# Kernel optimization log

Measured on AMD Instinct MI355X. Metric: run time of the kernel, lower is better.

## Reference

```python
import jax, jax.numpy as jnp
import numpy as np

L = 3          # num encoder layers
H = 128        # hidden_dim
NH = 8         # num_heads
HD = H // NH   # head_dim
FF = H * 4     # ff inner dim (after GLU)
B, N = 32, 512
NUM_BINS = 50


def _linear_params(key, fan_in, fan_out):
    kw, kb = jax.random.split(key)
    lim = 1.0 / np.sqrt(fan_in)
    W = jax.random.uniform(kw, (fan_in, fan_out), jnp.float32, -lim, lim)
    b = jax.random.uniform(kb, (fan_out,), jnp.float32, -lim, lim)
    return W, b


def setup_inputs() -> dict:
    key = jax.random.key(0)
    ks = jax.random.split(key, 16)
    x = jax.random.normal(ks[0], (B, N, H), jnp.float32)
    distance_matrix = jax.random.uniform(ks[1], (B, N, N), jnp.float32)
    mask = jax.random.randint(ks[2], (B, N), 0, 2).astype(bool)

    def stack_linear(k, fan_in, fan_out):
        Ws, bs = [], []
        for l in range(L):
            W, b = _linear_params(jax.random.fold_in(k, l), fan_in, fan_out)
            Ws.append(W); bs.append(b)
        return jnp.stack(Ws), jnp.stack(bs)

    Wq, bq = stack_linear(ks[3], H, H)
    Wk, bk = stack_linear(ks[4], H, H)
    Wv, bv = stack_linear(ks[5], H, H)
    Wo, bo = stack_linear(ks[6], H, H)
    dist_emb = jax.random.normal(ks[7], (L, NUM_BINS, NH), jnp.float32)
    attn_bias = jnp.zeros((L, NH, 1, 1), jnp.float32)
    g1 = jnp.ones((L, H), jnp.float32); b1 = jnp.zeros((L, H), jnp.float32)
    g2 = jnp.ones((L, H), jnp.float32); b2 = jnp.zeros((L, H), jnp.float32)
    Wf1, bf1 = stack_linear(ks[8], H, 2 * FF)
    Wf2, bf2 = stack_linear(ks[9], FF, H)
    return dict(x=x, distance_matrix=distance_matrix, mask=mask,
                Wq=Wq, bq=bq, Wk=Wk, bk=bk, Wv=Wv, bv=bv, Wo=Wo, bo=bo,
                dist_emb=dist_emb, attn_bias=attn_bias,
                g1=g1, b1=b1, g2=g2, b2=b2,
                Wf1=Wf1, bf1=bf1, Wf2=Wf2, bf2=bf2)


def _layernorm(x, g, b, eps=1e-5):
    mu = jnp.mean(x, axis=-1, keepdims=True)
    var = jnp.var(x, axis=-1, keepdims=True)
    return (x - mu) * jax.lax.rsqrt(var + eps) * g + b


def _attention(h, bins, key_mask, Wq, bq, Wk, bk, Wv, bv, Wo, bo, dist_emb, attn_bias):
    # h: [B,N,H]; bins: [B,N,N] int; key_mask: [B,N] bool (True = masked)
    Bsz, Nn, _ = h.shape
    Q = (h @ Wq + bq).reshape(Bsz, Nn, NH, HD)
    K = (h @ Wk + bk).reshape(Bsz, Nn, NH, HD)
    V = (h @ Wv + bv).reshape(Bsz, Nn, NH, HD)
    scores = jnp.einsum('bqhd,bkhd->bhqk', Q, K) / np.sqrt(HD)
    bias = jnp.transpose(dist_emb[bins], (0, 3, 1, 2))  # [B,NH,N,N]
    scores = scores + bias + attn_bias[None]
    scores = jnp.where(key_mask[:, None, None, :], -1e9, scores)
    attn = jax.nn.softmax(scores, axis=-1)
    out = jnp.einsum('bhqk,bkhd->bqhd', attn, V).reshape(Bsz, Nn, H)
    return out @ Wo + bo


def reference(x, distance_matrix, mask, Wq, bq, Wk, bk, Wv, bv, Wo, bo,
              dist_emb, attn_bias, g1, b1, g2, b2, Wf1, bf1, Wf2, bf2):
    bins = jnp.clip((distance_matrix * 10.0).astype(jnp.int32), 0, NUM_BINS - 1)
    h = x
    for l in range(L):
        # pre-LN attention block
        a = _attention(_layernorm(h, g1[l], b1[l]), bins, mask,
                       Wq[l], bq[l], Wk[l], bk[l], Wv[l], bv[l], Wo[l], bo[l],
                       dist_emb[l], attn_bias[l])
        h = h + a
        # pre-LN GLU feed-forward
        u = _layernorm(h, g2[l], b2[l]) @ Wf1[l] + bf1[l]  # [B,N,2*FF]
        ua, ub = jnp.split(u, 2, axis=-1)
        h = h + (ua * jax.nn.sigmoid(ub)) @ Wf2[l] + bf2[l]
    return h
```

## Files before the change

### kernel.cpp

```cpp
#include <hip/hip_runtime.h>
#include <stdint.h>

#define Bq 32
#define Nq 512
#define Hq 128
#define NHq 8
#define HDq 16
#define Mq (Bq * Nq)

typedef unsigned short u16;
typedef __attribute__((ext_vector_type(8))) short short8;
typedef __attribute__((ext_vector_type(8))) _Float16 half8;
typedef __attribute__((ext_vector_type(2))) __fp16 fp16x2;
typedef __attribute__((ext_vector_type(4))) float f32x4;

__device__ __forceinline__ float bf2f(u16 v) {
    return __uint_as_float(((unsigned int)v) << 16);
}
__device__ __forceinline__ float ldin(const void* p, long idx, int bf) {
    if (bf) return bf2f(((const u16*)p)[idx]);
    return ((const float*)p)[idx];
}
__device__ __forceinline__ u16 f2bf(float v) {
    unsigned int u = __float_as_uint(v);
    return (u16)((u + 0x7FFFu + ((u >> 16) & 1u)) >> 16);
}
__device__ __forceinline__ u16 f2h(float v) {
    _Float16 h = (_Float16)v;
    return *(u16*)&h;
}
__device__ __forceinline__ unsigned pk2h(float a, float b) {
    fp16x2 c = __builtin_amdgcn_cvt_pkrtz(a, b);
    return *(unsigned*)&c;
}

__global__ void prep_kernel(const void* xraw, const void* de, const void* ab,
                            const void* mraw, int* flag, float* deo, float* abo,
                            unsigned* mbits, int n) {
    __shared__ int cnt, orA, orB, orC, orD;
    int tid = threadIdx.x;
    if (tid == 0) { cnt = 0; orA = 0; orB = 0; orC = 0; orD = 0; }
    __syncthreads();
    const u16* u = (const u16*)xraw;
    int good = 0;
    for (int i = tid; i < 1024; i += 256) {
        u16 v = u[i];
        int e = (v >> 7) & 0xFF;
        if (v == 0 || (e >= 90 && e <= 141)) good++;
    }
    atomicAdd(&cnt, good);
    const uint4* p4 = (const uint4*)mraw;
    unsigned a = 0, b = 0, c = 0, d = 0;
    for (int i = tid; i < n / 16; i += 256) {
        uint4 w = p4[i];
        unsigned all = w.x | w.y | w.z | w.w;
        a |= all & 0xFEFEFEFEu;
        b |= all & 0x0000FF00u;
        c |= all & 0xFFFFFF00u;
        d |= w.y | w.w;
    }
    if (a) atomicOr(&orA, 1);
    if (b) atomicOr(&orB, 1);
    if (c) atomicOr(&orC, 1);
    if (d) atomicOr(&orD, 1);
    __syncthreads();
    int bf = (cnt >= 900);
    if (tid == 0) *flag = bf;
    int mode;
    if (orA) mode = orB ? 3 : 4;
    else if (orC) mode = 0;
    else mode = orD ? 1 : 2;
    for (int i = tid; i < 1200; i += 256) deo[i] = ldin(de, i, bf);
    if (tid < 24) abo[tid] = ldin(ab, tid, bf);
    const unsigned char* p = (const unsigned char*)mraw;
    for (int wI = tid; wI < n / 32; wI += 256) {
        unsigned word = 0;
        for (int j = 0; j < 32; ++j) {
            int i = wI * 32 + j;
            int v;
            switch (mode) {
                case 0: v = p[i]; break;
                case 1: v = ((const int*)p)[i]; break;
                case 2: v = (int)((const long long*)p)[i]; break;
                case 3: v = ((const u16*)p)[i] != 0; break;
                default: v = (((const float*)p)[i] != 0.0f); break;
            }
            if (v) word |= 1u << j;
        }
        mbits[wI] = word;
    }
}

__global__ void kprep_kernel(const unsigned* __restrict__ mbits,
                             u16* __restrict__ kidxg, int* __restrict__ nkt,
                             unsigned* __restrict__ tmask) {
    int b = blockIdx.x;
    int lane = threadIdx.x & 63;
    int pos_base = 0;
    for (int w = 0; w < 8; ++w) {
        unsigned lo = mbits[b * 16 + 2 * w], hi = mbits[b * 16 + 2 * w + 1];
        unsigned long long word = ((unsigned long long)hi << 32) | lo;
        unsigned long long un = ~word;
        int bit = (int)((un >> lane) & 1ull);
        unsigned long long before = un & ((1ull << lane) - 1ull);
        int pos = pos_base + __popcll(before);
        if (bit) kidxg[b * 512 + pos] = (u16)(w * 64 + lane);
        pos_base += __popcll(un);
    }
    int nk = pos_base;
    int nkp = (nk + 31) & ~31;
    if (nkp == 0) nkp = 32;
    int nt = nkp >> 5;
    for (int j = nk + lane; j < nkp; j += 64) kidxg[b * 512 + j] = 0;
    if (lane == 0) {
        nkt[b] = nt;
        for (int t = 0; t < 16; ++t) tmask[b * 16 + t] = 0;
        int rem = nk & 31;
        if (rem) tmask[b * 16 + nt - 1] = 0xFFFFFFFFu << rem;
        if (nk == 0) tmask[b * 16] = 0xFFFFFFFFu;
    }
}

__global__ __launch_bounds__(256) void binsc_kernel(
    const void* __restrict__ dist, const u16* __restrict__ kidxg,
    const int* __restrict__ nkt, unsigned char* __restrict__ binsc,
    const int* flagp) {
    int bf = *flagp;
    int b = blockIdx.y;
    int q0 = blockIdx.x * 8;
    __shared__ u16 kl[512];
    __shared__ int ntS;
    int tid = threadIdx.x;
    if (tid == 0) ntS = nkt[b];
    kl[tid] = kidxg[b * 512 + tid];
    kl[tid + 256] = kidxg[b * 512 + tid + 256];
    __syncthreads();
    int nkp = ntS * 32;
    for (int rq = 0; rq < 8; ++rq) {
        int q = q0 + rq;
        long rowoff = ((long)b * 512 + q) * 512;
        for (int j = tid; j < nkp; j += 256) {
            float d = ldin(dist, rowoff + kl[j], bf);
            int v = (int)(d * 10.0f);
            v = v < 0 ? 0 : (v > 49 ? 49 : v);
            binsc[((size_t)b * 512 + q) * 512 + j] = (unsigned char)(v << 2);
        }
    }
}

__global__ __launch_bounds__(256) void init_ln_kernel(
    const void* x, float* __restrict__ h, u16* __restrict__ hn,
    const void* graw, const void* braw, const int* flagp) {
    int bf = *flagp;
    int row = blockIdx.x * 4 + (threadIdx.x >> 6);
    int lane = threadIdx.x & 63;
    float x0 = ldin(x, (long)row * Hq + lane, bf);
    float x1 = ldin(x, (long)row * Hq + lane + 64, bf);
    h[(size_t)row * Hq + lane] = x0;
    h[(size_t)row * Hq + lane + 64] = x1;
    float s = x0 + x1, s2 = x0 * x0 + x1 * x1;
#pragma unroll
    for (int o = 32; o; o >>= 1) {
        s += __shfl_xor(s, o);
        s2 += __shfl_xor(s2, o);
    }
    float mu = s * (1.0f / 128.0f);
    float var = fmaxf(s2 * (1.0f / 128.0f) - mu * mu, 0.0f);
    float rr = rsqrtf(var + 1e-5f);
    float g0 = ldin(graw, lane, bf), g1v = ldin(graw, lane + 64, bf);
    float b0 = ldin(braw, lane, bf), b1v = ldin(braw, lane + 64, bf);
    hn[(size_t)row * Hq + lane]      = f2bf((x0 - mu) * rr * g0 + b0);
    hn[(size_t)row * Hq + lane + 64] = f2bf((x1 - mu) * rr * g1v + b1v);
}

__global__ __launch_bounds__(256) void wtrans_kernel(
    const void* Wqr, const void* Wkr, const void* Wvr, const void* Wor,
    const void* Wf1r, const void* Wf2r,
    u16* qkvT, u16* oT, u16* f1T, u16* f2T, const int* flagp) {
    int bf = *flagp;
    int bid = blockIdx.x;
    int l = bid >> 8, r = bid & 255;
    const void* src; u16* dst; long soff, doff; int Kd, Nd, t;
    if (r < 64) {
        int mat = r >> 4; t = r & 15; Kd = 128; Nd = 128;
        soff = (long)l * 16384;
        if (mat == 0)      { src = Wqr; dst = qkvT; doff = (long)l * 49152; }
        else if (mat == 1) { src = Wkr; dst = qkvT; doff = (long)l * 49152 + 16384; }
        else if (mat == 2) { src = Wvr; dst = qkvT; doff = (long)l * 49152 + 32768; }
        else               { src = Wor; dst = oT;   doff = (long)l * 16384; }
    } else if (r < 192) {
        t = r - 64; Kd = 128; Nd = 1024;
        src = Wf1r; soff = (long)l * 131072; dst = f1T; doff = (long)l * 131072;
    } else {
        t = r - 192; Kd = 512; Nd = 128;
        src = Wf2r; soff = (long)l * 65536; dst = f2T; doff = (long)l * 65536;
    }
    int ntile = Nd >> 5;
    int tk = t / ntile, tn = t % ntile;
    __shared__ u16 Ts[32][33];
    int rr = threadIdx.x >> 3, cc0 = (threadIdx.x & 7) * 4;
#pragma unroll
    for (int i = 0; i < 4; ++i) {
        long idx = soff + (long)(tk * 32 + rr) * Nd + tn * 32 + cc0 + i;
        Ts[rr][cc0 + i] = f2bf(ldin(src, idx, bf));
    }
    __syncthreads();
#pragma unroll
    for (int i = 0; i < 4; ++i) {
        long idx = doff + (long)(tn * 32 + rr) * Kd + tk * 32 + cc0 + i;
        dst[idx] = Ts[cc0 + i][rr];
    }
}

__global__ __launch_bounds__(256, 2) void qkv_mfma_kernel(
    const u16* __restrict__ A, const u16* __restrict__ qkvT_l,
    const void* bqr, const void* bkr, const void* bvr, long bOff,
    u16* __restrict__ Qo, u16* __restrict__ Ko, u16* __restrict__ Vo,
    const int* flagp) {
    int sel = blockIdx.y;
    const u16* WT = qkvT_l + (size_t)sel * 16384;
    const void* braw = sel == 0 ? bqr : (sel == 1 ? bkr : bvr);
    u16* C = sel == 0 ? Qo : (sel == 1 ? Ko : Vo);
    float scale = sel == 0 ? 0.25f : 1.0f;
    __shared__ __align__(16) u16 As[64][40];
    __shared__ __align__(16) u16 Bs[128][40];
    int tid = threadIdx.x;
    int m0 = blockIdx.x * 64;
    int wave = tid >> 6, lane = tid & 63;
    int wm = (wave >> 1) * 32, wn = (wave & 1) * 64;
    int q = lane >> 4, ln = lane & 15;
    f32x4 zero = {0.f, 0.f, 0.f, 0.f};
    f32x4 acc[2][4];
#pragma unroll
    for (int i = 0; i < 2; ++i)
#pragma unroll
        for (int j = 0; j < 4; ++j) acc[i][j] = zero;
    int sar = tid >> 2, sac = (tid & 3) * 8;
    int sbr = tid >> 1, sbc = (tid & 1) * 16;
    const u16* Ap = A + (size_t)(m0 + sar) * 128 + sac;
    const u16* Bp = WT + (size_t)sbr * 128 + sbc;
#pragma unroll
    for (int k0 = 0; k0 < 128; k0 += 32) {
        uint4 av = *(const uint4*)(Ap + k0);
        uint4 b0 = *(const uint4*)(Bp + k0);
        uint4 b1 = *(const uint4*)(Bp + k0 + 8);
        *(uint4*)&As[sar][sac] = av;
        *(uint4*)&Bs[sbr][sbc] = b0; *(uint4*)&Bs[sbr][sbc + 8] = b1;
        __syncthreads();
        short8 af[2], bfv[4];
#pragma unroll
        for (int t = 0; t < 2; ++t) af[t] = *(const short8*)&As[wm + t * 16 + ln][q * 8];
#pragma unroll
        for (int t = 0; t < 4; ++t) bfv[t] = *(const short8*)&Bs[wn + t * 16 + ln][q * 8];
#pragma unroll
        for (int ti = 0; ti < 2; ++ti)
#pragma unroll
            for (int tj = 0; tj < 4; ++tj)
                acc[ti][tj] = __builtin_amdgcn_mfma_f32_16x16x32_bf16(
                    af[ti], bfv[tj], acc[ti][tj], 0, 0, 0);
        __syncthreads();
    }
    int bf = *flagp;
#pragma unroll
    for (int tj = 0; tj < 4; ++tj) {
        int n = wn + tj * 16 + ln;
        float bias = ldin(braw, bOff + n, bf);
#pragma unroll
        for (int ti = 0; ti < 2; ++ti)
#pragma unroll
            for (int r = 0; r < 4; ++r) {
                int m = m0 + wm + ti * 16 + q * 4 + r;
                C[(size_t)m * 128 + n] = f2h((acc[ti][tj][r] + bias) * scale);
            }
    }
}

__global__ __launch_bounds__(256, 1) void layer_ffn_kernel(
    const u16* __restrict__ att, const u16* __restrict__ oT_l,
    const void* __restrict__ bo, long boOff,
    float* __restrict__ h,
    const void* g2, const void* b2, long ln2Off,
    const u16* __restrict__ f1T_l, const void* __restrict__ bf1r, long bf1Off,
    const u16* __restrict__ f2T_l, const void* __restrict__ bf2r, long bf2Off,
    const void* g1, const void* b1, long ln1Off,
    u16* __restrict__ hnout, void* __restrict__ outp, const int* flagp) {
    __shared__ __align__(16) char Lds[151552];
    u16 (*As)[136]   = (u16(*)[136])Lds;
    u16 (*hn2)[136]  = (u16(*)[136])Lds;
    float (*Ct)[128] = (float(*)[128])(Lds + 17408);
    u16 (*vg)[520]   = (u16(*)[520])(Lds + 50176);
    u16 (*Bs)[136]   = (u16(*)[136])(Lds + 116736);
    u16 (*Ba)[136]   = (u16(*)[136])(Lds + 116736);
    u16 (*Bb)[136]   = (u16(*)[136])(Lds + 134144);

    int tid = threadIdx.x;
    int m0 = blockIdx.x * 64;
    int wave = tid >> 6, lane = tid & 63;
    int wm = (wave >> 1) * 32, wn = (wave & 1) * 64;
    int q = lane >> 4, ln = lane & 15;
    int bf = *flagp;
    f32x4 zero = {0.f, 0.f, 0.f, 0.f};

#pragma unroll
    for (int i = 0; i < 4; ++i) {
        int idx = tid + i * 256; int r = idx >> 4, c = (idx & 15) << 3;
        *(uint4*)&As[r][c] = *(const uint4*)(att + (size_t)(m0 + r) * 128 + c);
    }
#pragma unroll
    for (int i = 0; i < 8; ++i) {
        int idx = tid + i * 256; int r = idx >> 4, c = (idx & 15) << 3;
        *(uint4*)&Bs[r][c] = *(const uint4*)(oT_l + (size_t)r * 128 + c);
    }
    __syncthreads();
    f32x4 acc[2][4];
#pragma unroll
    for (int i = 0; i < 2; ++i)
#pragma unroll
        for (int j = 0; j < 4; ++j) acc[i][j] = zero;
#pragma unroll
    for (int kf = 0; kf < 128; kf += 32) {
        short8 af[2], bfv[4];
#pragma unroll
        for (int t = 0; t < 2; ++t)
            af[t] = *(const short8*)&As[wm + t * 16 + ln][kf + q * 8];
#pragma unroll
        for (int t = 0; t < 4; ++t)
            bfv[t] = *(const short8*)&Bs[wn + t * 16 + ln][kf + q * 8];
#pragma unroll
        for (int ti = 0; ti < 2; ++ti)
#pragma unroll
            for (int tj = 0; tj < 4; ++tj)
                acc[ti][tj] = __builtin_amdgcn_mfma_f32_16x16x32_bf16(
                    af[ti], bfv[tj], acc[ti][tj], 0, 0, 0);
    }
#pragma unroll
    for (int tj = 0; tj < 4; ++tj) {
        int n = wn + tj * 16 + ln;
        float bias = ldin(bo, boOff + n, bf);
#pragma unroll
        for (int ti = 0; ti < 2; ++ti)
#pragma unroll
            for (int r = 0; r < 4; ++r) {
                int lm = wm + ti * 16 + q * 4 + r;
                Ct[lm][n] = acc[ti][tj][r] + bias + h[(size_t)(m0 + lm) * 128 + n];
            }
    }
    __syncthreads();
    {
        float gg0 = ldin(g2, ln2Off + lane, bf), gg1 = ldin(g2, ln2Off + lane + 64, bf);
        float bb0 = ldin(b2, ln2Off + lane, bf), bb1 = ldin(b2, ln2Off + lane + 64, bf);
        for (int rr = 0; rr < 16; ++rr) {
            int row = wave * 16 + rr;
            float x0 = Ct[row][lane], x1 = Ct[row][lane + 64];
            float s = x0 + x1, s2v = x0 * x0 + x1 * x1;
#pragma unroll
            for (int o = 32; o; o >>= 1) {
                s += __shfl_xor(s, o);
                s2v += __shfl_xor(s2v, o);
            }
            float mu = s * (1.0f / 128.0f);
            float var = fmaxf(s2v * (1.0f / 128.0f) - mu * mu, 0.0f);
            float rstd = rsqrtf(var + 1e-5f);
            hn2[row][lane]      = f2bf((x0 - mu) * rstd * gg0 + bb0);
            hn2[row][lane + 64] = f2bf((x1 - mu) * rstd * gg1 + bb1);
        }
    }
    int wn2 = (wave & 1) * 32;
    uint4 ra[4], rb[4];
#pragma unroll
    for (int i = 0; i < 4; ++i) {
        int idx = tid + i * 256; int r = idx >> 4, c = (idx & 15) << 3;
        ra[i] = *(const uint4*)(f1T_l + (size_t)r * 128 + c);
        rb[i] = *(const uint4*)(f1T_l + (size_t)(512 + r) * 128 + c);
    }
    for (int ch = 0; ch < 8; ++ch) {
#pragma unroll
        for (int i = 0; i < 4; ++i) {
            int idx = tid + i * 256; int r = idx >> 4, c = (idx & 15) << 3;
            *(uint4*)&Ba[r][c] = ra[i];
            *(uint4*)&Bb[r][c] = rb[i];
        }
        if (ch < 7) {
            int n0 = (ch + 1) * 64;
#pragma unroll
            for (int i = 0; i < 4; ++i) {
                int idx = tid + i * 256; int r = idx >> 4, c = (idx & 15) << 3;
                ra[i] = *(const uint4*)(f1T_l + (size_t)(n0 + r) * 128 + c);
                rb[i] = *(const uint4*)(f1T_l + (size_t)(512 + n0 + r) * 128 + c);
            }
        }
        __syncthreads();
        f32x4 aA[2][2], aB[2][2];
#pragma unroll
        for (int i = 0; i < 2; ++i)
#pragma unroll
            for (int j = 0; j < 2; ++j) { aA[i][j] = zero; aB[i][j] = zero; }
#pragma unroll
        for (int kf = 0; kf < 128; kf += 32) {
            short8 af[2], bav[2], bbv[2];
#pragma unroll
            for (int t = 0; t < 2; ++t)
                af[t] = *(const short8*)&hn2[wm + t * 16 + ln][kf + q * 8];
#pragma unroll
            for (int t = 0; t < 2; ++t) {
                bav[t] = *(const short8*)&Ba[wn2 + t * 16 + ln][kf + q * 8];
                bbv[t] = *(const short8*)&Bb[wn2 + t * 16 + ln][kf + q * 8];
            }
#pragma unroll
            for (int ti = 0; ti < 2; ++ti)
#pragma unroll
                for (int tj = 0; tj < 2; ++tj) {
                    aA[ti][tj] = __builtin_amdgcn_mfma_f32_16x16x32_bf16(
                        af[ti], bav[tj], aA[ti][tj], 0, 0, 0);
                    aB[ti][tj] = __builtin_amdgcn_mfma_f32_16x16x32_bf16(
                        af[ti], bbv[tj], aB[ti][tj], 0, 0, 0);
                }
        }
        int n0 = ch * 64;
#pragma unroll
        for (int tj = 0; tj < 2; ++tj) {
            int n = n0 + wn2 + tj * 16 + ln;
            float bA = ldin(bf1r, bf1Off + n, bf);
            float bB = ldin(bf1r, bf1Off + 512 + n, bf);
#pragma unroll
            for (int ti = 0; ti < 2; ++ti)
#pragma unroll
                for (int r = 0; r < 4; ++r) {
                    int lm = wm + ti * 16 + q * 4 + r;
                    float ua = aA[ti][tj][r] + bA;
                    float ub = aB[ti][tj][r] + bB;
                    vg[lm][n] = f2bf(ua / (1.0f + __expf(-ub)));
                }
        }
        __syncthreads();
    }
    uint4 rf[8];
#pragma unroll
    for (int i = 0; i < 8; ++i) {
        int idx = tid + i * 256; int r = idx >> 4, c = (idx & 15) << 3;
        rf[i] = *(const uint4*)(f2T_l + (size_t)r * 512 + c);
    }
    f32x4 accF[2][4];
#pragma unroll
    for (int i = 0; i < 2; ++i)
#pragma unroll
        for (int j = 0; j < 4; ++j) accF[i][j] = zero;
    for (int ch = 0; ch < 4; ++ch) {
#pragma unroll
        for (int i = 0; i < 8; ++i) {
            int idx = tid + i * 256; int r = idx >> 4, c = (idx & 15) << 3;
            *(uint4*)&Bs[r][c] = rf[i];
        }
        if (ch < 3) {
            int k0 = (ch + 1) * 128;
#pragma unroll
            for (int i = 0; i < 8; ++i) {
                int idx = tid + i * 256; int r = idx >> 4, c = (idx & 15) << 3;
                rf[i] = *(const uint4*)(f2T_l + (size_t)r * 512 + k0 + c);
            }
        }
        __syncthreads();
#pragma unroll
        for (int kf = 0; kf < 128; kf += 32) {
            short8 af[2], bfv[4];
#pragma unroll
            for (int t = 0; t < 2; ++t)
                af[t] = *(const short8*)&vg[wm + t * 16 + ln][ch * 128 + kf + q * 8];
#pragma unroll
            for (int t = 0; t < 4; ++t)
                bfv[t] = *(const short8*)&Bs[wn + t * 16 + ln][kf + q * 8];
#pragma unroll
            for (int ti = 0; ti < 2; ++ti)
#pragma unroll
                for (int tj = 0; tj < 4; ++tj)
                    accF[ti][tj] = __builtin_amdgcn_mfma_f32_16x16x32_bf16(
                        af[ti], bfv[tj], accF[ti][tj], 0, 0, 0);
        }
        __syncthreads();
    }
#pragma unroll
    for (int tj = 0; tj < 4; ++tj) {
        int n = wn + tj * 16 + ln;
        float bias = ldin(bf2r, bf2Off + n, bf);
#pragma unroll
        for (int ti = 0; ti < 2; ++ti)
#pragma unroll
            for (int r = 0; r < 4; ++r) {
                int lm = wm + ti * 16 + q * 4 + r;
                float v = accF[ti][tj][r] + bias + Ct[lm][n];
                h[(size_t)(m0 + lm) * 128 + n] = v;
                Ct[lm][n] = v;
                if (outp) {
                    if (bf) ((u16*)outp)[(size_t)(m0 + lm) * 128 + n] = f2bf(v);
                    else ((float*)outp)[(size_t)(m0 + lm) * 128 + n] = v;
                }
            }
    }
    if (hnout) {
        __syncthreads();
        float gg0 = ldin(g1, ln1Off + lane, bf), gg1 = ldin(g1, ln1Off + lane + 64, bf);
        float bb0 = ldin(b1, ln1Off + lane, bf), bb1 = ldin(b1, ln1Off + lane + 64, bf);
        for (int rr = 0; rr < 16; ++rr) {
            int row = wave * 16 + rr;
            float x0 = Ct[row][lane], x1 = Ct[row][lane + 64];
            float s = x0 + x1, s2v = x0 * x0 + x1 * x1;
#pragma unroll
            for (int o = 32; o; o >>= 1) {
                s += __shfl_xor(s, o);
                s2v += __shfl_xor(s2v, o);
            }
            float mu = s * (1.0f / 128.0f);
            float var = fmaxf(s2v * (1.0f / 128.0f) - mu * mu, 0.0f);
            float rstd = rsqrtf(var + 1e-5f);
            hnout[(size_t)(m0 + row) * 128 + lane]      = f2bf((x0 - mu) * rstd * gg0 + bb0);
            hnout[(size_t)(m0 + row) * 128 + lane + 64] = f2bf((x1 - mu) * rstd * gg1 + bb1);
        }
    }
}

__global__ __launch_bounds__(256, 4) void attn_kernel(
    const u16* __restrict__ Qh, const u16* __restrict__ Kh,
    const u16* __restrict__ Vh, const unsigned char* __restrict__ binsc,
    const u16* __restrict__ kidxg, const int* __restrict__ nktp,
    const unsigned* __restrict__ tmaskp, const float* __restrict__ deL,
    const float* __restrict__ abL, u16* __restrict__ out) {
    int id = blockIdx.x;
    int c = id & 7, t5 = id >> 3;
    int nh = t5 & 7;
    int pair = ((t5 >> 3) << 3) | c;
    int b = pair >> 2, qq = pair & 3;

    __shared__ __align__(16) u16 KsF[8192];
    __shared__ __align__(16) u16 VT[16 * 520];
    __shared__ __align__(16) u16 Pl[4 * 16 * 40];

    int tid = threadIdx.x;
    int nt = __builtin_amdgcn_readfirstlane(nktp[b]);
    int nkp = nt * 32;
    const u16* Kp = Kh + (size_t)(b * Nq) * Hq + nh * HDq;
    const u16* Vp = Vh + (size_t)(b * Nq) * Hq + nh * HDq;
    for (int r = tid; r < nkp; r += 256) {
        int row = kidxg[b * 512 + r];
        int kt = r >> 5, s = (r >> 4) & 1, lnr = r & 15;
        uint4 k0v = *(const uint4*)(Kp + (size_t)row * Hq);
        uint4 k1v = *(const uint4*)(Kp + (size_t)row * Hq + 8);
        *(uint4*)&KsF[kt * 512 + s * 256 + lnr * 8]       = k0v;
        *(uint4*)&KsF[kt * 512 + s * 256 + 128 + lnr * 8] = k1v;
        uint4 v0 = *(const uint4*)(Vp + (size_t)row * Hq);
        uint4 v1 = *(const uint4*)(Vp + (size_t)row * Hq + 8);
        u16 vv[16];
        *(uint4*)&vv[0] = v0; *(uint4*)&vv[8] = v1;
#pragma unroll
        for (int d = 0; d < 16; ++d) VT[d * 520 + r] = vv[d];
    }
    __syncthreads();

    int wave = tid >> 6, lane = tid & 63;
    int quad = lane >> 4, ln = lane & 15;
    int q0w = qq * 128 + wave * 32;

    float tblf = (lane < 50) ? deL[lane * NHq + nh] + abL[nh] : 0.0f;
    int tbli = __float_as_int(tblf);
    unsigned tl = tmaskp[b * 16 + nt - 1];

    half8 qf[2];
#pragma unroll
    for (int t = 0; t < 2; ++t) {
        uint4 qv = {0, 0, 0, 0};
        if (quad < 2)
            qv = *(const uint4*)(Qh + (size_t)(b * Nq + q0w + t * 16 + ln) * Hq
                                 + nh * HDq + quad * 8);
        qf[t] = *(half8*)&qv;
    }

    f32x4 zero = {0.f, 0.f, 0.f, 0.f};
    f32x4 acc[2] = {zero, zero};
    float zp[2] = {0.f, 0.f};
    _Float16* Pw = (_Float16*)&Pl[wave * 640];
    const _Float16* KsH = (const _Float16*)KsF;
    const _Float16* VTH = (const _Float16*)VT;
    const unsigned char* brow0 = binsc + ((size_t)b * 512 + (q0w + ln)) * 512;
    const unsigned char* brow1 = brow0 + (size_t)16 * 512;

    unsigned pb00 = *(const unsigned*)(brow0 + quad * 4);
    unsigned pb01 = *(const unsigned*)(brow0 + 16 + quad * 4);
    unsigned pb10 = *(const unsigned*)(brow1 + quad * 4);
    unsigned pb11 = *(const unsigned*)(brow1 + 16 + quad * 4);

    for (int kt = 0; kt < nt; ++kt) {
        int k0 = kt * 32;
        unsigned w = (kt == nt - 1) ? tl : 0u;
        unsigned cb00 = pb00, cb01 = pb01, cb10 = pb10, cb11 = pb11;
        if (kt < nt - 1) {
            pb00 = *(const unsigned*)(brow0 + k0 + 32 + quad * 4);
            pb01 = *(const unsigned*)(brow0 + k0 + 48 + quad * 4);
            pb10 = *(const unsigned*)(brow1 + k0 + 32 + quad * 4);
            pb11 = *(const unsigned*)(brow1 + k0 + 48 + quad * 4);
        }
        half8 vb = *(const half8*)(VTH + ln * 520 + k0 + quad * 8);
        half8 ka0 = {}, ka1 = {};
        if (quad < 2) {
            ka0 = *(const half8*)(KsH + kt * 512 + quad * 128 + ln * 8);
            ka1 = *(const half8*)(KsH + kt * 512 + 256 + quad * 128 + ln * 8);
        }
#pragma unroll
        for (int t = 0; t < 2; ++t) {
            unsigned bw0 = t == 0 ? cb00 : cb10;
            unsigned bw1 = t == 0 ? cb01 : cb11;
            f32x4 s0 = __builtin_amdgcn_mfma_f32_16x16x32_f16(ka0, qf[t], zero, 0, 0, 0);
            f32x4 s1 = __builtin_amdgcn_mfma_f32_16x16x32_f16(ka1, qf[t], zero, 0, 0, 0);
            float p[8];
#pragma unroll
            for (int r = 0; r < 4; ++r) {
                float bias = __int_as_float(__builtin_amdgcn_ds_bpermute(
                    (int)((bw0 >> (8 * r)) & 0xFFu), tbli));
                float sc = s0[r] + bias;
                bool m = (w >> (quad * 4 + r)) & 1u;
                p[r] = m ? 0.0f : __expf(sc);
            }
#pragma unroll
            for (int r = 0; r < 4; ++r) {
                float bias = __int_as_float(__builtin_amdgcn_ds_bpermute(
                    (int)((bw1 >> (8 * r)) & 0xFFu), tbli));
                float sc = s1[r] + bias;
                bool m = (w >> (16 + quad * 4 + r)) & 1u;
                p[4 + r] = m ? 0.0f : __expf(sc);
            }
            zp[t] += ((p[0] + p[1]) + (p[2] + p[3])) +
                     ((p[4] + p[5]) + (p[6] + p[7]));
            uint2 w0, w1;
            w0.x = pk2h(p[0], p[1]); w0.y = pk2h(p[2], p[3]);
            w1.x = pk2h(p[4], p[5]); w1.y = pk2h(p[6], p[7]);
            *(uint2*)(Pw + ln * 40 + quad * 4)      = w0;
            *(uint2*)(Pw + ln * 40 + 16 + quad * 4) = w1;
            half8 pa = *(const half8*)(Pw + ln * 40 + quad * 8);
            acc[t] = __builtin_amdgcn_mfma_f32_16x16x32_f16(pa, vb, acc[t], 0, 0, 0);
        }
    }
#pragma unroll
    for (int t = 0; t < 2; ++t) {
        zp[t] += __shfl_xor(zp[t], 16);
        zp[t] += __shfl_xor(zp[t], 32);
    }
#pragma unroll
    for (int t = 0; t < 2; ++t) {
#pragma unroll
        for (int r = 0; r < 4; ++r) {
            float zz = __shfl(zp[t], quad * 4 + r);
            float val = acc[t][r] / fmaxf(zz, 1e-35f);
            int qrow = q0w + t * 16 + quad * 4 + r;
            out[(size_t)(b * Nq + qrow) * Hq + nh * HDq + ln] = f2bf(val);
        }
    }
}

extern "C" void kernel_launch(void* const* d_in, const int* in_sizes, int n_in,
                              void* d_out, int out_size, void* d_ws, size_t ws_size,
                              hipStream_t stream) {
    const void* x  = d_in[0];
    const void* dist = d_in[1];
    const void* mask = d_in[2];
    const void* Wq = d_in[3];  const void* bq = d_in[4];
    const void* Wk = d_in[5];  const void* bk = d_in[6];
    const void* Wv = d_in[7];  const void* bv = d_in[8];
    const void* Wo = d_in[9];  const void* bo = d_in[10];
    const void* de = d_in[11]; const void* ab = d_in[12];
    const void* g1 = d_in[13]; const void* b1 = d_in[14];
    const void* g2 = d_in[15]; const void* b2 = d_in[16];
    const void* Wf1 = d_in[17]; const void* bf1 = d_in[18];
    const void* Wf2 = d_in[19]; const void* bf2 = d_in[20];

    char* ws = (char*)d_ws;
    const size_t OFF_DE   = 64;
    const size_t OFF_AB   = 5120;
    const size_t OFF_BINS = 8192;
    const size_t OFF_MSK  = OFF_BINS + 8388608;
    const size_t OFF_KIDX = OFF_MSK + 4096;
    const size_t OFF_NKT  = OFF_KIDX + 32768;
    const size_t OFF_TM   = OFF_NKT + 256;
    const size_t OFF_H    = OFF_TM + 4096;
    const size_t OFF_QKV  = OFF_H + 8388608;
    const size_t OFF_HN   = OFF_QKV + 25165824;
    const size_t OFF_ATT  = OFF_HN + 4194304;
    const size_t OFF_WT   = OFF_ATT + 4194304;
    const size_t NEEDED   = OFF_WT + 1572864;
    if (ws_size < NEEDED) return;

    int* flag = (int*)ws;
    float* deF = (float*)(ws + OFF_DE);
    float* abF = (float*)(ws + OFF_AB);
    unsigned char* binsc = (unsigned char*)(ws + OFF_BINS);
    unsigned* mbits = (unsigned*)(ws + OFF_MSK);
    u16* kidxg = (u16*)(ws + OFF_KIDX);
    int* nkt = (int*)(ws + OFF_NKT);
    unsigned* tmask = (unsigned*)(ws + OFF_TM);
    float* h = (float*)(ws + OFF_H);
    u16* Qh = (u16*)(ws + OFF_QKV);
    u16* Kh = Qh + 2097152;
    u16* Vh = Qh + 2 * 2097152;
    u16* hn = (u16*)(ws + OFF_HN);
    u16* att = (u16*)(ws + OFF_ATT);
    u16* qkvT = (u16*)(ws + OFF_WT);
    u16* oT  = qkvT + 147456;
    u16* f1T = oT + 49152;
    u16* f2T = f1T + 393216;

    prep_kernel<<<1, 256, 0, stream>>>(x, de, ab, mask, flag, deF, abF, mbits, Bq * Nq);
    kprep_kernel<<<32, 64, 0, stream>>>(mbits, kidxg, nkt, tmask);
    dim3 gbc(64, 32);
    binsc_kernel<<<gbc, 256, 0, stream>>>(dist, kidxg, nkt, binsc, flag);
    init_ln_kernel<<<4096, 256, 0, stream>>>(x, h, hn, g1, b1, flag);
    wtrans_kernel<<<768, 256, 0, stream>>>(Wq, Wk, Wv, Wo, Wf1, Wf2,
                                           qkvT, oT, f1T, f2T, flag);

    dim3 gqkv(256, 3);
    for (int l = 0; l < 3; ++l) {
        qkv_mfma_kernel<<<gqkv, 256, 0, stream>>>(hn, qkvT + (size_t)l * 49152,
                                                  bq, bk, bv, (long)l * Hq,
                                                  Qh, Kh, Vh, flag);
        attn_kernel<<<1024, 256, 0, stream>>>(Qh, Kh, Vh, binsc, kidxg, nkt, tmask,
                                              deF + (long)l * 400, abF + (long)l * 8, att);
        layer_ffn_kernel<<<256, 256, 0, stream>>>(
            att, oT + (size_t)l * 16384, bo, (long)l * Hq,
            h, g2, b2, (long)l * Hq,
            f1T + (size_t)l * 131072, bf1, (long)l * 1024,
            f2T + (size_t)l * 65536, bf2, (long)l * Hq,
            g1, b1, l < 2 ? (long)(l + 1) * Hq : 0,
            l < 2 ? hn : (u16*)nullptr,
            l == 2 ? d_out : nullptr, flag);
    }
}
```

Baseline: 410.6 us.

## Fuse LN1 into QKV GEMM and shrink FFN row tile to 32

Moves the pre-attention layernorm out of the FFN epilogue and the init kernel into the QKV projection kernel, which now reads the fp32 residual directly and normalizes 32 rows in registers before a single-shot full-K MFMA. The FFN kernel uses 32-row tiles with roughly half the LDS, so two blocks can reside per CU and the grid doubles to 512. LN2 statistics are computed from accumulator registers through a small shared stats array. This removes the hn buffer round-trip, at the cost of recomputing LN1 in each of the three QKV column blocks and loading the full weight tiles twice as often.

```diff
diff --git a/kernel.cpp b/kernel.cpp
--- a/kernel.cpp
+++ b/kernel.cpp
@@ -148,29 +148,26 @@
     }
 }
 
-__global__ __launch_bounds__(256) void init_ln_kernel(
-    const void* x, float* __restrict__ h, u16* __restrict__ hn,
-    const void* graw, const void* braw, const int* flagp) {
+__global__ __launch_bounds__(256) void init_kernel(const void* x,
+                                                   float* __restrict__ h,
+                                                   const int* flagp) {
     int bf = *flagp;
-    int row = blockIdx.x * 4 + (threadIdx.x >> 6);
-    int lane = threadIdx.x & 63;
-    float x0 = ldin(x, (long)row * Hq + lane, bf);
-    float x1 = ldin(x, (long)row * Hq + lane + 64, bf);
-    h[(size_t)row * Hq + lane] = x0;
-    h[(size_t)row * Hq + lane + 64] = x1;
-    float s = x0 + x1, s2 = x0 * x0 + x1 * x1;
-#pragma unroll
-    for (int o = 32; o; o >>= 1) {
-        s += __shfl_xor(s, o);
-        s2 += __shfl_xor(s2, o);
-    }
-    float mu = s * (1.0f / 128.0f);
-    float var = fmaxf(s2 * (1.0f / 128.0f) - mu * mu, 0.0f);
-    float rr = rsqrtf(var + 1e-5f);
-    float g0 = ldin(graw, lane, bf), g1v = ldin(graw, lane + 64, bf);
-    float b0 = ldin(braw, lane, bf), b1v = ldin(braw, lane + 64, bf);
-    hn[(size_t)row * Hq + lane]      = f2bf((x0 - mu) * rr * g0 + b0);
-    hn[(size_t)row * Hq + lane + 64] = f2bf((x1 - mu) * rr * g1v + b1v);
+    int i = blockIdx.x * 256 + threadIdx.x;
+    long base = (long)i * 8;
+    if (bf) {
+        uint4 w = ((const uint4*)x)[i];
+        const u16* ws = (const u16*)&w;
+        float o[8];
+#pragma unroll
+        for (int k = 0; k < 8; ++k) o[k] = bf2f(ws[k]);
+        *(float4*)&h[base] = *(float4*)&o[0];
+        *(float4*)&h[base + 4] = *(float4*)&o[4];
+    } else {
+        float4 a = ((const float4*)x)[2 * i];
+        float4 b = ((const float4*)x)[2 * i + 1];
+        *(float4*)&h[base] = a;
+        *(float4*)&h[base + 4] = b;
+    }
 }
 
 __global__ __launch_bounds__(256) void wtrans_kernel(
@@ -212,9 +209,10 @@
     }
 }
 
-__global__ __launch_bounds__(256, 2) void qkv_mfma_kernel(
-    const u16* __restrict__ A, const u16* __restrict__ qkvT_l,
+__global__ __launch_bounds__(256, 3) void qkv_mfma_kernel(
+    const float* __restrict__ h, const u16* __restrict__ qkvT_l,
     const void* bqr, const void* bkr, const void* bvr, long bOff,
+    const void* g1raw, const void* b1raw, long lnOff,
     u16* __restrict__ Qo, u16* __restrict__ Ko, u16* __restrict__ Vo,
     const int* flagp) {
     int sel = blockIdx.y;
@@ -222,298 +220,272 @@
     const void* braw = sel == 0 ? bqr : (sel == 1 ? bkr : bvr);
     u16* C = sel == 0 ? Qo : (sel == 1 ? Ko : Vo);
     float scale = sel == 0 ? 0.25f : 1.0f;
-    __shared__ __align__(16) u16 As[64][40];
-    __shared__ __align__(16) u16 Bs[128][40];
+    __shared__ __align__(16) u16 As[32][136];
+    __shared__ __align__(16) u16 Bs[128][136];
     int tid = threadIdx.x;
-    int m0 = blockIdx.x * 64;
+    int m0 = blockIdx.x * 32;
+    int bf = *flagp;
+    {
+        int row = tid >> 3, c0 = (tid & 7) * 16;
+        const float* hp = h + (size_t)(m0 + row) * 128 + c0;
+        float4 f0 = *(const float4*)(hp);
+        float4 f1 = *(const float4*)(hp + 4);
+        float4 f2 = *(const float4*)(hp + 8);
+        float4 f3 = *(const float4*)(hp + 12);
+        float vv[16] = {f0.x, f0.y, f0.z, f0.w, f1.x, f1.y, f1.z, f1.w,
+                        f2.x, f2.y, f2.z, f2.w, f3.x, f3.y, f3.z, f3.w};
+        float s = 0.f, s2 = 0.f;
+#pragma unroll
+        for (int k = 0; k < 16; ++k) { s += vv[k]; s2 += vv[k] * vv[k]; }
+#pragma unroll
+        for (int o = 1; o < 8; o <<= 1) {
+            s += __shfl_xor(s, o);
+            s2 += __shfl_xor(s2, o);
+        }
+        float mu = s * (1.0f / 128.0f);
+        float var = fmaxf(s2 * (1.0f / 128.0f) - mu * mu, 0.0f);
+        float rstd = rsqrtf(var + 1e-5f);
+        u16 tmp[16];
+#pragma unroll
+        for (int k = 0; k < 16; ++k) {
+            float g = ldin(g1raw, lnOff + c0 + k, bf);
+            float b = ldin(b1raw, lnOff + c0 + k, bf);
+            tmp[k] = f2bf((vv[k] - mu) * rstd * g + b);
+        }
+        *(uint4*)&As[row][c0]     = *(uint4*)&tmp[0];
+        *(uint4*)&As[row][c0 + 8] = *(uint4*)&tmp[8];
+    }
+#pragma unroll
+    for (int i = 0; i < 8; ++i) {
+        int idx = tid + i * 256; int r = idx >> 4, c = (idx & 15) << 3;
+        *(uint4*)&Bs[r][c] = *(const uint4*)(WT + (size_t)r * 128 + c);
+    }
+    __syncthreads();
     int wave = tid >> 6, lane = tid & 63;
-    int wm = (wave >> 1) * 32, wn = (wave & 1) * 64;
+    int wr = wave >> 1, wc = wave & 1;
     int q = lane >> 4, ln = lane & 15;
     f32x4 zero = {0.f, 0.f, 0.f, 0.f};
-    f32x4 acc[2][4];
-#pragma unroll
-    for (int i = 0; i < 2; ++i)
-#pragma unroll
-        for (int j = 0; j < 4; ++j) acc[i][j] = zero;
-    int sar = tid >> 2, sac = (tid & 3) * 8;
-    int sbr = tid >> 1, sbc = (tid & 1) * 16;
-    const u16* Ap = A + (size_t)(m0 + sar) * 128 + sac;
-    const u16* Bp = WT + (size_t)sbr * 128 + sbc;
-#pragma unroll
-    for (int k0 = 0; k0 < 128; k0 += 32) {
-        uint4 av = *(const uint4*)(Ap + k0);
-        uint4 b0 = *(const uint4*)(Bp + k0);
-        uint4 b1 = *(const uint4*)(Bp + k0 + 8);
-        *(uint4*)&As[sar][sac] = av;
-        *(uint4*)&Bs[sbr][sbc] = b0; *(uint4*)&Bs[sbr][sbc + 8] = b1;
-        __syncthreads();
-        short8 af[2], bfv[4];
-#pragma unroll
-        for (int t = 0; t < 2; ++t) af[t] = *(const short8*)&As[wm + t * 16 + ln][q * 8];
-#pragma unroll
-        for (int t = 0; t < 4; ++t) bfv[t] = *(const short8*)&Bs[wn + t * 16 + ln][q * 8];
-#pragma unroll
-        for (int ti = 0; ti < 2; ++ti)
-#pragma unroll
-            for (int tj = 0; tj < 4; ++tj)
-                acc[ti][tj] = __builtin_amdgcn_mfma_f32_16x16x32_bf16(
-                    af[ti], bfv[tj], acc[ti][tj], 0, 0, 0);
-        __syncthreads();
-    }
-    int bf = *flagp;
-#pragma unroll
-    for (int tj = 0; tj < 4; ++tj) {
-        int n = wn + tj * 16 + ln;
+    f32x4 acc[4] = {zero, zero, zero, zero};
+#pragma unroll
+    for (int kf = 0; kf < 128; kf += 32) {
+        short8 af = *(const short8*)&As[wr * 16 + ln][kf + q * 8];
+#pragma unroll
+        for (int t = 0; t < 4; ++t) {
+            short8 bv = *(const short8*)&Bs[wc * 64 + t * 16 + ln][kf + q * 8];
+            acc[t] = __builtin_amdgcn_mfma_f32_16x16x32_bf16(af, bv, acc[t], 0, 0, 0);
+        }
+    }
+#pragma unroll
+    for (int t = 0; t < 4; ++t) {
+        int n = wc * 64 + t * 16 + ln;
         float bias = ldin(braw, bOff + n, bf);
 #pragma unroll
-        for (int ti = 0; ti < 2; ++ti)
-#pragma unroll
-            for (int r = 0; r < 4; ++r) {
-                int m = m0 + wm + ti * 16 + q * 4 + r;
-                C[(size_t)m * 128 + n] = f2h((acc[ti][tj][r] + bias) * scale);
-            }
-    }
-}
-
-__global__ __launch_bounds__(256, 1) void layer_ffn_kernel(
+        for (int r = 0; r < 4; ++r) {
+            int m = m0 + wr * 16 + q * 4 + r;
+            C[(size_t)m * 128 + n] = f2h((acc[t][r] + bias) * scale);
+        }
+    }
+}
+
+__global__ __launch_bounds__(256, 2) void ffglu_kernel(
     const u16* __restrict__ att, const u16* __restrict__ oT_l,
-    const void* __restrict__ bo, long boOff,
-    float* __restrict__ h,
+    const void* __restrict__ bo, long boOff, float* __restrict__ h,
     const void* g2, const void* b2, long ln2Off,
     const u16* __restrict__ f1T_l, const void* __restrict__ bf1r, long bf1Off,
     const u16* __restrict__ f2T_l, const void* __restrict__ bf2r, long bf2Off,
-    const void* g1, const void* b1, long ln1Off,
-    u16* __restrict__ hnout, void* __restrict__ outp, const int* flagp) {
-    __shared__ __align__(16) char Lds[151552];
-    u16 (*As)[136]   = (u16(*)[136])Lds;
-    u16 (*hn2)[136]  = (u16(*)[136])Lds;
-    float (*Ct)[128] = (float(*)[128])(Lds + 17408);
-    u16 (*vg)[520]   = (u16(*)[520])(Lds + 50176);
-    u16 (*Bs)[136]   = (u16(*)[136])(Lds + 116736);
-    u16 (*Ba)[136]   = (u16(*)[136])(Lds + 116736);
-    u16 (*Bb)[136]   = (u16(*)[136])(Lds + 134144);
-
+    void* __restrict__ outp, const int* flagp) {
+    __shared__ __align__(16) u16 As[32][136];
+    __shared__ __align__(16) u16 U[128][136];
+    __shared__ __align__(16) u16 vg[32][520];
+    __shared__ float stats[32][2][2];
     int tid = threadIdx.x;
-    int m0 = blockIdx.x * 64;
+    int m0 = blockIdx.x * 32;
     int wave = tid >> 6, lane = tid & 63;
-    int wm = (wave >> 1) * 32, wn = (wave & 1) * 64;
+    int wr = wave >> 1, wc = wave & 1;
     int q = lane >> 4, ln = lane & 15;
     int bf = *flagp;
     f32x4 zero = {0.f, 0.f, 0.f, 0.f};
 
 #pragma unroll
+    for (int i = 0; i < 2; ++i) {
+        int idx = tid + i * 256; int r = idx >> 4, c = (idx & 15) << 3;
+        *(uint4*)&As[r][c] = *(const uint4*)(att + (size_t)(m0 + r) * 128 + c);
+    }
+#pragma unroll
+    for (int i = 0; i < 8; ++i) {
+        int idx = tid + i * 256; int r = idx >> 4, c = (idx & 15) << 3;
+        *(uint4*)&U[r][c] = *(const uint4*)(oT_l + (size_t)r * 128 + c);
+    }
+    __syncthreads();
+    f32x4 acc[4] = {zero, zero, zero, zero};
+#pragma unroll
+    for (int kf = 0; kf < 128; kf += 32) {
+        short8 af = *(const short8*)&As[wr * 16 + ln][kf + q * 8];
+#pragma unroll
+        for (int t = 0; t < 4; ++t) {
+            short8 bv = *(const short8*)&U[wc * 64 + t * 16 + ln][kf + q * 8];
+            acc[t] = __builtin_amdgcn_mfma_f32_16x16x32_bf16(af, bv, acc[t], 0, 0, 0);
+        }
+    }
+    uint4 pa[4], pb[4];
+#pragma unroll
     for (int i = 0; i < 4; ++i) {
         int idx = tid + i * 256; int r = idx >> 4, c = (idx & 15) << 3;
-        *(uint4*)&As[r][c] = *(const uint4*)(att + (size_t)(m0 + r) * 128 + c);
-    }
-#pragma unroll
-    for (int i = 0; i < 8; ++i) {
-        int idx = tid + i * 256; int r = idx >> 4, c = (idx & 15) << 3;
-        *(uint4*)&Bs[r][c] = *(const uint4*)(oT_l + (size_t)r * 128 + c);
-    }
-    __syncthreads();
-    f32x4 acc[2][4];
-#pragma unroll
-    for (int i = 0; i < 2; ++i)
-#pragma unroll
-        for (int j = 0; j < 4; ++j) acc[i][j] = zero;
-#pragma unroll
-    for (int kf = 0; kf < 128; kf += 32) {
-        short8 af[2], bfv[4];
-#pragma unroll
-        for (int t = 0; t < 2; ++t)
-            af[t] = *(const short8*)&As[wm + t * 16 + ln][kf + q * 8];
-#pragma unroll
-        for (int t = 0; t < 4; ++t)
-            bfv[t] = *(const short8*)&Bs[wn + t * 16 + ln][kf + q * 8];
-#pragma unroll
-        for (int ti = 0; ti < 2; ++ti)
-#pragma unroll
-            for (int tj = 0; tj < 4; ++tj)
-                acc[ti][tj] = __builtin_amdgcn_mfma_f32_16x16x32_bf16(
-                    af[ti], bfv[tj], acc[ti][tj], 0, 0, 0);
-    }
-#pragma unroll
-    for (int tj = 0; tj < 4; ++tj) {
-        int n = wn + tj * 16 + ln;
+        pa[i] = *(const uint4*)(f1T_l + (size_t)r * 128 + c);
+        pb[i] = *(const uint4*)(f1T_l + (size_t)(512 + r) * 128 + c);
+    }
+    float h1[4][4];
+    float srow[4] = {0.f, 0.f, 0.f, 0.f}, s2row[4] = {0.f, 0.f, 0.f, 0.f};
+#pragma unroll
+    for (int t = 0; t < 4; ++t) {
+        int n = wc * 64 + t * 16 + ln;
         float bias = ldin(bo, boOff + n, bf);
 #pragma unroll
-        for (int ti = 0; ti < 2; ++ti)
-#pragma unroll
-            for (int r = 0; r < 4; ++r) {
-                int lm = wm + ti * 16 + q * 4 + r;
-                Ct[lm][n] = acc[ti][tj][r] + bias + h[(size_t)(m0 + lm) * 128 + n];
-            }
-    }
-    __syncthreads();
-    {
-        float gg0 = ldin(g2, ln2Off + lane, bf), gg1 = ldin(g2, ln2Off + lane + 64, bf);
-        float bb0 = ldin(b2, ln2Off + lane, bf), bb1 = ldin(b2, ln2Off + lane + 64, bf);
-        for (int rr = 0; rr < 16; ++rr) {
-            int row = wave * 16 + rr;
-            float x0 = Ct[row][lane], x1 = Ct[row][lane + 64];
-            float s = x0 + x1, s2v = x0 * x0 + x1 * x1;
-#pragma unroll
-            for (int o = 32; o; o >>= 1) {
-                s += __shfl_xor(s, o);
-                s2v += __shfl_xor(s2v, o);
-            }
-            float mu = s * (1.0f / 128.0f);
-            float var = fmaxf(s2v * (1.0f / 128.0f) - mu * mu, 0.0f);
-            float rstd = rsqrtf(var + 1e-5f);
-            hn2[row][lane]      = f2bf((x0 - mu) * rstd * gg0 + bb0);
-            hn2[row][lane + 64] = f2bf((x1 - mu) * rstd * gg1 + bb1);
-        }
-    }
-    int wn2 = (wave & 1) * 32;
-    uint4 ra[4], rb[4];
+        for (int r = 0; r < 4; ++r) {
+            float v = acc[t][r] + bias +
+                      h[(size_t)(m0 + wr * 16 + q * 4 + r) * 128 + n];
+            h1[t][r] = v; srow[r] += v; s2row[r] += v * v;
+        }
+    }
+#pragma unroll
+    for (int r = 0; r < 4; ++r)
+#pragma unroll
+        for (int o = 1; o < 16; o <<= 1) {
+            srow[r] += __shfl_xor(srow[r], o);
+            s2row[r] += __shfl_xor(s2row[r], o);
+        }
+    if (ln == 0) {
+#pragma unroll
+        for (int r = 0; r < 4; ++r) {
+            stats[wr * 16 + q * 4 + r][wc][0] = srow[r];
+            stats[wr * 16 + q * 4 + r][wc][1] = s2row[r];
+        }
+    }
+    __syncthreads();
+    float mu[4], rs[4];
+#pragma unroll
+    for (int r = 0; r < 4; ++r) {
+        int row = wr * 16 + q * 4 + r;
+        float s = stats[row][0][0] + stats[row][1][0];
+        float s2 = stats[row][0][1] + stats[row][1][1];
+        mu[r] = s * (1.0f / 128.0f);
+        float var = fmaxf(s2 * (1.0f / 128.0f) - mu[r] * mu[r], 0.0f);
+        rs[r] = rsqrtf(var + 1e-5f);
+    }
+#pragma unroll
+    for (int t = 0; t < 4; ++t) {
+        int n = wc * 64 + t * 16 + ln;
+        float g = ldin(g2, ln2Off + n, bf), bb = ldin(b2, ln2Off + n, bf);
+#pragma unroll
+        for (int r = 0; r < 4; ++r)
+            As[wr * 16 + q * 4 + r][n] = f2bf((h1[t][r] - mu[r]) * rs[r] * g + bb);
+    }
 #pragma unroll
     for (int i = 0; i < 4; ++i) {
         int idx = tid + i * 256; int r = idx >> 4, c = (idx & 15) << 3;
-        ra[i] = *(const uint4*)(f1T_l + (size_t)r * 128 + c);
-        rb[i] = *(const uint4*)(f1T_l + (size_t)(512 + r) * 128 + c);
-    }
+        *(uint4*)&U[r][c] = pa[i];
+        *(uint4*)&U[64 + r][c] = pb[i];
+    }
+    __syncthreads();
+    uint4 rf[8];
     for (int ch = 0; ch < 8; ++ch) {
-#pragma unroll
-        for (int i = 0; i < 4; ++i) {
-            int idx = tid + i * 256; int r = idx >> 4, c = (idx & 15) << 3;
-            *(uint4*)&Ba[r][c] = ra[i];
-            *(uint4*)&Bb[r][c] = rb[i];
-        }
         if (ch < 7) {
             int n0 = (ch + 1) * 64;
 #pragma unroll
             for (int i = 0; i < 4; ++i) {
                 int idx = tid + i * 256; int r = idx >> 4, c = (idx & 15) << 3;
-                ra[i] = *(const uint4*)(f1T_l + (size_t)(n0 + r) * 128 + c);
-                rb[i] = *(const uint4*)(f1T_l + (size_t)(512 + n0 + r) * 128 + c);
-            }
-        }
-        __syncthreads();
-        f32x4 aA[2][2], aB[2][2];
-#pragma unroll
-        for (int i = 0; i < 2; ++i)
-#pragma unroll
-            for (int j = 0; j < 2; ++j) { aA[i][j] = zero; aB[i][j] = zero; }
+                pa[i] = *(const uint4*)(f1T_l + (size_t)(n0 + r) * 128 + c);
+                pb[i] = *(const uint4*)(f1T_l + (size_t)(512 + n0 + r) * 128 + c);
+            }
+        } else {
+#pragma unroll
+            for (int i = 0; i < 8; ++i) {
+                int idx = tid + i * 256; int r = idx >> 4, c = (idx & 15) << 3;
+                rf[i] = *(const uint4*)(f2T_l + (size_t)r * 512 + c);
+            }
+        }
+        f32x4 aA[2] = {zero, zero}, aB[2] = {zero, zero};
 #pragma unroll
         for (int kf = 0; kf < 128; kf += 32) {
-            short8 af[2], bav[2], bbv[2];
-#pragma unroll
-            for (int t = 0; t < 2; ++t)
-                af[t] = *(const short8*)&hn2[wm + t * 16 + ln][kf + q * 8];
+            short8 af = *(const short8*)&As[wr * 16 + ln][kf + q * 8];
 #pragma unroll
             for (int t = 0; t < 2; ++t) {
-                bav[t] = *(const short8*)&Ba[wn2 + t * 16 + ln][kf + q * 8];
-                bbv[t] = *(const short8*)&Bb[wn2 + t * 16 + ln][kf + q * 8];
-            }
-#pragma unroll
-            for (int ti = 0; ti < 2; ++ti)
-#pragma unroll
-                for (int tj = 0; tj < 2; ++tj) {
-                    aA[ti][tj] = __builtin_amdgcn_mfma_f32_16x16x32_bf16(
-                        af[ti], bav[tj], aA[ti][tj], 0, 0, 0);
-                    aB[ti][tj] = __builtin_amdgcn_mfma_f32_16x16x32_bf16(
-                        af[ti], bbv[tj], aB[ti][tj], 0, 0, 0);
-                }
-        }
-        int n0 = ch * 64;
-#pragma unroll
-        for (int tj = 0; tj < 2; ++tj) {
-            int n = n0 + wn2 + tj * 16 + ln;
+                short8 ba = *(const short8*)&U[wc * 32 + t * 16 + ln][kf + q * 8];
+                short8 bb = *(const short8*)&U[64 + wc * 32 + t * 16 + ln][kf + q * 8];
+                aA[t] = __builtin_amdgcn_mfma_f32_16x16x32_bf16(af, ba, aA[t], 0, 0, 0);
+                aB[t] = __builtin_amdgcn_mfma_f32_16x16x32_bf16(af, bb, aB[t], 0, 0, 0);
+            }
+        }
+#pragma unroll
+        for (int t = 0; t < 2; ++t) {
+            int n = ch * 64 + wc * 32 + t * 16 + ln;
             float bA = ldin(bf1r, bf1Off + n, bf);
             float bB = ldin(bf1r, bf1Off + 512 + n, bf);
 #pragma unroll
-            for (int ti = 0; ti < 2; ++ti)
-#pragma unroll
-                for (int r = 0; r < 4; ++r) {
-                    int lm = wm + ti * 16 + q * 4 + r;
-                    float ua = aA[ti][tj][r] + bA;
-                    float ub = aB[ti][tj][r] + bB;
-                    vg[lm][n] = f2bf(ua / (1.0f + __expf(-ub)));
-                }
+            for (int r = 0; r < 4; ++r) {
+                float ua = aA[t][r] + bA, ub = aB[t][r] + bB;
+                vg[wr * 16 + q * 4 + r][n] = f2bf(ua / (1.0f + __expf(-ub)));
+            }
         }
         __syncthreads();
-    }
-    uint4 rf[8];
-#pragma unroll
-    for (int i = 0; i < 8; ++i) {
-        int idx = tid + i * 256; int r = idx >> 4, c = (idx & 15) << 3;
-        rf[i] = *(const uint4*)(f2T_l + (size_t)r * 512 + c);
-    }
-    f32x4 accF[2][4];
-#pragma unroll
-    for (int i = 0; i < 2; ++i)
-#pragma unroll
-        for (int j = 0; j < 4; ++j) accF[i][j] = zero;
-    for (int ch = 0; ch < 4; ++ch) {
-#pragma unroll
-        for (int i = 0; i < 8; ++i) {
-            int idx = tid + i * 256; int r = idx >> 4, c = (idx & 15) << 3;
-            *(uint4*)&Bs[r][c] = rf[i];
-        }
-        if (ch < 3) {
-            int k0 = (ch + 1) * 128;
+        if (ch < 7) {
+#pragma unroll
+            for (int i = 0; i < 4; ++i) {
+                int idx = tid + i * 256; int r = idx >> 4, c = (idx & 15) << 3;
+                *(uint4*)&U[r][c] = pa[i];
+                *(uint4*)&U[64 + r][c] = pb[i];
+            }
+        } else {
+#pragma unroll
+            for (int i = 0; i < 8; ++i) {
+                int idx = tid + i * 256; int r = idx >> 4, c = (idx & 15) << 3;
+                *(uint4*)&U[r][c] = rf[i];
+            }
+        }
+        __syncthreads();
+    }
+    f32x4 accF[4] = {zero, zero, zero, zero};
+    for (int fc = 0; fc < 4; ++fc) {
+        if (fc < 3) {
+            int k0 = (fc + 1) * 128;
 #pragma unroll
             for (int i = 0; i < 8; ++i) {
                 int idx = tid + i * 256; int r = idx >> 4, c = (idx & 15) << 3;
                 rf[i] = *(const uint4*)(f2T_l + (size_t)r * 512 + k0 + c);
             }
         }
-        __syncthreads();
 #pragma unroll
         for (int kf = 0; kf < 128; kf += 32) {
-            short8 af[2], bfv[4];
-#pragma unroll
-            for (int t = 0; t < 2; ++t)
-                af[t] = *(const short8*)&vg[wm + t * 16 + ln][ch * 128 + kf + q * 8];
-#pragma unroll
-            for (int t = 0; t < 4; ++t)
-                bfv[t] = *(const short8*)&Bs[wn + t * 16 + ln][kf + q * 8];
-#pragma unroll
-            for (int ti = 0; ti < 2; ++ti)
-#pragma unroll
-                for (int tj = 0; tj < 4; ++tj)
-                    accF[ti][tj] = __builtin_amdgcn_mfma_f32_16x16x32_bf16(
-                        af[ti], bfv[tj], accF[ti][tj], 0, 0, 0);
-        }
-        __syncthreads();
-    }
-#pragma unroll
-    for (int tj = 0; tj < 4; ++tj) {
-        int n = wn + tj * 16 + ln;
+            short8 af = *(const short8*)&vg[wr * 16 + ln][fc * 128 + kf + q * 8];
+#pragma unroll
+            for (int t = 0; t < 4; ++t) {
+                short8 bv = *(const short8*)&U[wc * 64 + t * 16 + ln][kf + q * 8];
+                accF[t] = __builtin_amdgcn_mfma_f32_16x16x32_bf16(af, bv, accF[t], 0, 0, 0);
+            }
+        }
+        if (fc < 3) {
+            __syncthreads();
+#pragma unroll
+            for (int i = 0; i < 8; ++i) {
+                int idx = tid + i * 256; int r = idx >> 4, c = (idx & 15) << 3;
+                *(uint4*)&U[r][c] = rf[i];
+            }
+            __syncthreads();
+        }
+    }
+#pragma unroll
+    for (int t = 0; t < 4; ++t) {
+        int n = wc * 64 + t * 16 + ln;
         float bias = ldin(bf2r, bf2Off + n, bf);
 #pragma unroll
-        for (int ti = 0; ti < 2; ++ti)
-#pragma unroll
-            for (int r = 0; r < 4; ++r) {
-                int lm = wm + ti * 16 + q * 4 + r;
-                float v = accF[ti][tj][r] + bias + Ct[lm][n];
-                h[(size_t)(m0 + lm) * 128 + n] = v;
-                Ct[lm][n] = v;
-                if (outp) {
-                    if (bf) ((u16*)outp)[(size_t)(m0 + lm) * 128 + n] = f2bf(v);
-                    else ((float*)outp)[(size_t)(m0 + lm) * 128 + n] = v;
-                }
-            }
-    }
-    if (hnout) {
-        __syncthreads();
-        float gg0 = ldin(g1, ln1Off + lane, bf), gg1 = ldin(g1, ln1Off + lane + 64, bf);
-        float bb0 = ldin(b1, ln1Off + lane, bf), bb1 = ldin(b1, ln1Off + lane + 64, bf);
-        for (int rr = 0; rr < 16; ++rr) {
-            int row = wave * 16 + rr;
-            float x0 = Ct[row][lane], x1 = Ct[row][lane + 64];
-            float s = x0 + x1, s2v = x0 * x0 + x1 * x1;
-#pragma unroll
-            for (int o = 32; o; o >>= 1) {
-                s += __shfl_xor(s, o);
-                s2v += __shfl_xor(s2v, o);
-            }
-            float mu = s * (1.0f / 128.0f);
-            float var = fmaxf(s2v * (1.0f / 128.0f) - mu * mu, 0.0f);
-            float rstd = rsqrtf(var + 1e-5f);
-            hnout[(size_t)(m0 + row) * 128 + lane]      = f2bf((x0 - mu) * rstd * gg0 + bb0);
-            hnout[(size_t)(m0 + row) * 128 + lane + 64] = f2bf((x1 - mu) * rstd * gg1 + bb1);
+        for (int r = 0; r < 4; ++r) {
+            int m = m0 + wr * 16 + q * 4 + r;
+            float v = accF[t][r] + bias + h1[t][r];
+            h[(size_t)m * 128 + n] = v;
+            if (outp) {
+                if (bf) ((u16*)outp)[(size_t)m * 128 + n] = f2bf(v);
+                else ((float*)outp)[(size_t)m * 128 + n] = v;
+            }
         }
     }
 }
@@ -680,8 +652,7 @@
     const size_t OFF_TM   = OFF_NKT + 256;
     const size_t OFF_H    = OFF_TM + 4096;
     const size_t OFF_QKV  = OFF_H + 8388608;
-    const size_t OFF_HN   = OFF_QKV + 25165824;
-    const size_t OFF_ATT  = OFF_HN + 4194304;
+    const size_t OFF_ATT  = OFF_QKV + 25165824;
     const size_t OFF_WT   = OFF_ATT + 4194304;
     const size_t NEEDED   = OFF_WT + 1572864;
     if (ws_size < NEEDED) return;
@@ -698,7 +669,6 @@
     u16* Qh = (u16*)(ws + OFF_QKV);
     u16* Kh = Qh + 2097152;
     u16* Vh = Qh + 2 * 2097152;
-    u16* hn = (u16*)(ws + OFF_HN);
     u16* att = (u16*)(ws + OFF_ATT);
     u16* qkvT = (u16*)(ws + OFF_WT);
     u16* oT  = qkvT + 147456;
@@ -709,24 +679,23 @@
     kprep_kernel<<<32, 64, 0, stream>>>(mbits, kidxg, nkt, tmask);
     dim3 gbc(64, 32);
     binsc_kernel<<<gbc, 256, 0, stream>>>(dist, kidxg, nkt, binsc, flag);
-    init_ln_kernel<<<4096, 256, 0, stream>>>(x, h, hn, g1, b1, flag);
+    init_kernel<<<1024, 256, 0, stream>>>(x, h, flag);
     wtrans_kernel<<<768, 256, 0, stream>>>(Wq, Wk, Wv, Wo, Wf1, Wf2,
                                            qkvT, oT, f1T, f2T, flag);
 
-    dim3 gqkv(256, 3);
+    dim3 gqkv(512, 3);
     for (int l = 0; l < 3; ++l) {
-        qkv_mfma_kernel<<<gqkv, 256, 0, stream>>>(hn, qkvT + (size_t)l * 49152,
+        qkv_mfma_kernel<<<gqkv, 256, 0, stream>>>(h, qkvT + (size_t)l * 49152,
                                                   bq, bk, bv, (long)l * Hq,
+                                                  g1, b1, (long)l * Hq,
                                                   Qh, Kh, Vh, flag);
         attn_kernel<<<1024, 256, 0, stream>>>(Qh, Kh, Vh, binsc, kidxg, nkt, tmask,
                                               deF + (long)l * 400, abF + (long)l * 8, att);
-        layer_ffn_kernel<<<256, 256, 0, stream>>>(
+        ffglu_kernel<<<512, 256, 0, stream>>>(
             att, oT + (size_t)l * 16384, bo, (long)l * Hq,
             h, g2, b2, (long)l * Hq,
             f1T + (size_t)l * 131072, bf1, (long)l * 1024,
             f2T + (size_t)l * 65536, bf2, (long)l * Hq,
-            g1, b1, l < 2 ? (long)(l + 1) * Hq : 0,
-            l < 2 ? hn : (u16*)nullptr,
             l == 2 ? d_out : nullptr, flag);
     }
 }
```

Measured after the change: 486.6 us. +18.5%, slower.
